# Optimization experiments

Measured on AMD Instinct MI355X. Metric: run time of the kernel, lower is better.

## Reference

```python
import jax, jax.numpy as jnp
import numpy as np

HEADS = 16
KERNEL_EPS = 1e-4  # performer_pytorch softmax_kernel eps
LN_EPS = 1e-5


def layernorm(x, g, b):
    m = jnp.mean(x, axis=-1, keepdims=True)
    v = jnp.var(x, axis=-1, keepdims=True)
    return (x - m) * jax.lax.rsqrt(v + LN_EPS) * g + b


def softmax_kernel(x, proj, is_query):
    # FAVOR+ positive random features (performer_pytorch softmax_kernel)
    d = x.shape[-1]
    m = proj.shape[0]
    xn = x * (d ** -0.25)                                   # data_normalizer * data
    dd = jnp.einsum('bhnd,md->bhnm', xn, proj)              # projected logits
    diag = 0.5 * jnp.sum(xn * xn, axis=-1, keepdims=True)   # ||x||^2/2 * normalizer^2
    if is_query:
        stab = jnp.max(dd, axis=-1, keepdims=True)
    else:
        stab = jnp.max(dd, axis=(-2, -1), keepdims=True)
    return (m ** -0.5) * (jnp.exp(dd - diag - stab) + KERNEL_EPS)


def favor_attention(x, proj, Wq, bq, Wk, bk, Wv, bv, Wo, bo):
    B, N, D = x.shape
    dh = D // HEADS

    def split(t):
        return t.reshape(B, N, HEADS, dh).transpose(0, 2, 1, 3)  # b h n d

    q = split(x @ Wq.T + bq)
    k = split(x @ Wk.T + bk)
    v = split(x @ Wv.T + bv)

    qp = softmax_kernel(q, proj, True)    # b h n m
    kp = softmax_kernel(k, proj, False)   # b h n m

    # non-causal linear attention: O(n*m*d)
    ksum = kp.sum(axis=2)                                    # b h m
    d_inv = 1.0 / jnp.einsum('bhnm,bhm->bhn', qp, ksum)      # b h n
    ctx = jnp.einsum('bhnm,bhnd->bhmd', kp, v)               # b h m d
    out = jnp.einsum('bhnm,bhmd,bhn->bhnd', qp, ctx, d_inv)  # b h n d

    out = out.transpose(0, 2, 1, 3).reshape(B, N, D)
    return out @ Wo.T + bo


def reference(x, proj, ln1_g, ln1_b, Wq, bq, Wk, bk, Wv, bv, Wo, bo,
              ln2_g, ln2_b, W1, b1, W2, b2):
    depth = proj.shape[0]
    for i in range(depth):
        h = layernorm(x, ln1_g[i], ln1_b[i])
        x = x + favor_attention(h, proj[i], Wq[i], bq[i], Wk[i], bk[i],
                                Wv[i], bv[i], Wo[i], bo[i])
        h = layernorm(x, ln2_g[i], ln2_b[i])
        x = x + (jax.nn.gelu(h @ W1[i].T + b1[i], approximate=False) @ W2[i].T + b2[i])
    return x


def _orthogonal_features(rng, m, d):
    # gaussian orthogonal random matrix, scaling=1 (rows scaled by sqrt(d))
    blocks = []
    for _ in range(m // d):
        qmat, _ = np.linalg.qr(rng.standard_normal((d, d)))
        blocks.append(qmat.T)
    return (np.sqrt(d) * np.concatenate(blocks, axis=0)).astype(np.float32)


def setup_inputs() -> dict:
    B, N, D, L, M, DH = 4, 2048, 1024, 4, 256, 64
    key = jax.random.key(0)
    ks = jax.random.split(key, 8)
    rng = np.random.default_rng(0)
    proj = jnp.asarray(np.stack([_orthogonal_features(rng, M, DH) for _ in range(L)]))
    s = 0.02
    return {
        'x': jax.random.normal(ks[0], (B, N, D), jnp.float32),
        'proj': proj,
        'ln1_g': jnp.ones((L, D), jnp.float32),
        'ln1_b': jnp.zeros((L, D), jnp.float32),
        'Wq': s * jax.random.normal(ks[1], (L, D, D), jnp.float32),
        'bq': jnp.zeros((L, D), jnp.float32),
        'Wk': s * jax.random.normal(ks[2], (L, D, D), jnp.float32),
        'bk': jnp.zeros((L, D), jnp.float32),
        'Wv': s * jax.random.normal(ks[3], (L, D, D), jnp.float32),
        'bv': jnp.zeros((L, D), jnp.float32),
        'Wo': s * jax.random.normal(ks[4], (L, D, D), jnp.float32),
        'bo': jnp.zeros((L, D), jnp.float32),
        'ln2_g': jnp.ones((L, D), jnp.float32),
        'ln2_b': jnp.zeros((L, D), jnp.float32),
        'W1': s * jax.random.normal(ks[5], (L, D, D), jnp.float32),
        'b1': jnp.zeros((L, D), jnp.float32),
        'W2': s * jax.random.normal(ks[6], (L, D, D), jnp.float32),
        'b2': jnp.zeros((L, D), jnp.float32),
    }
```

## Files before the change

kernel.cpp:

```cpp
#include <hip/hip_runtime.h>

#define B_    4
#define N_    2048
#define D_    1024
#define L_    4
#define M_    256
#define DH_   64
#define H_    16
#define BH_   64
#define ROWS_ 8192
#define WN_   1048576

typedef __bf16 bf16x8 __attribute__((ext_vector_type(8)));
typedef float  f32x4  __attribute__((ext_vector_type(4)));
typedef unsigned short u16;

__device__ __forceinline__ u16 f2b(float f){
  unsigned u = __float_as_uint(f);
  u += 0x7FFFu + ((u >> 16) & 1u);
  return (u16)(u >> 16);
}
__device__ __forceinline__ float b2f(u16 h){ return __uint_as_float(((unsigned)h) << 16); }

__device__ __forceinline__ void gload16(const u16* g, u16* l){
  __builtin_amdgcn_global_load_lds(
      (const __attribute__((address_space(1))) void*)g,
      (__attribute__((address_space(3))) void*)l, 16, 0, 0);
}

__global__ __launch_bounds__(256) void wcvt_k(const float* __restrict__ s, u16* __restrict__ d, long n){
  long i = ((long)blockIdx.x*256 + threadIdx.x)*4;
  if (i+3 < n){
    float4 v = *(const float4*)(s+i);
    d[i]=f2b(v.x); d[i+1]=f2b(v.y); d[i+2]=f2b(v.z); d[i+3]=f2b(v.w);
  } else {
    for(long j=i;j<n;j++) d[j]=f2b(s[j]);
  }
}

__global__ __launch_bounds__(256) void wcvt6_k(
    const float* __restrict__ s0, const float* __restrict__ s1,
    const float* __restrict__ s2, const float* __restrict__ s3,
    const float* __restrict__ s4, const float* __restrict__ s5,
    u16* __restrict__ dbase)
{
  int ty = blockIdx.y;
  const float* s = (ty==0)?s0:(ty==1)?s1:(ty==2)?s2:(ty==3)?s3:(ty==4)?s4:s5;
  long i = ((long)blockIdx.x*256 + threadIdx.x)*4;
  float4 v = *(const float4*)(s+i);
  long l = i >> 20, j = i & (WN_-1);
  u16* d = dbase + l*(6l*WN_) + (long)ty*WN_ + j;
  d[0]=f2b(v.x); d[1]=f2b(v.y); d[2]=f2b(v.z); d[3]=f2b(v.w);
}

__global__ void fillf_k(float* o, long n, float v){
  long i=(long)blockIdx.x*256+threadIdx.x; if(i<n) o[i]=v;
}

__global__ __launch_bounds__(256) void ln_k(const float* __restrict__ x,
    const float* __restrict__ g, const float* __restrict__ bt, u16* __restrict__ h){
  int row = blockIdx.x, t = threadIdx.x;
  const float* xr = x + (long)row*D_;
  float4 v = *(const float4*)(xr + t*4);
  float s  = v.x+v.y+v.z+v.w;
  float ss = v.x*v.x+v.y*v.y+v.z*v.z+v.w*v.w;
  #pragma unroll
  for (int m=1;m<64;m<<=1){ s += __shfl_xor(s,m); ss += __shfl_xor(ss,m); }
  __shared__ float ps[4][2];
  int w=t>>6;
  if ((t&63)==0){ ps[w][0]=s; ps[w][1]=ss; }
  __syncthreads();
  s  = ps[0][0]+ps[1][0]+ps[2][0]+ps[3][0];
  ss = ps[0][1]+ps[1][1]+ps[2][1]+ps[3][1];
  float mean = s*(1.0f/D_);
  float rs = rsqrtf(ss*(1.0f/D_) - mean*mean + 1e-5f);
  int c=t*4;
  u16* hr = h + (long)row*D_;
  hr[c+0]=f2b((v.x-mean)*rs*g[c+0]+bt[c+0]);
  hr[c+1]=f2b((v.y-mean)*rs*g[c+1]+bt[c+1]);
  hr[c+2]=f2b((v.z-mean)*rs*g[c+2]+bt[c+2]);
  hr[c+3]=f2b((v.w-mean)*rs*g[c+3]+bt[c+3]);
}

#define LOAD_PF(pF, P, w, lr, lg) \
  _Pragma("unroll") \
  for (int ni=0;ni<4;ni++) \
    _Pragma("unroll") \
    for (int ks=0;ks<2;ks++) \
      pF[ni][ks] = *(const bf16x8*)((P) + ((w)*64+ni*16+(lr))*64 + ks*32 + (lg)*8);

#define STAGE_XS_DG(Xs, X, b, hh, n0, dgL) \
  _Pragma("unroll") \
  for (int i=0;i<2;i++){ \
    int c=threadIdx.x+i*256, row=c>>3, c8=c&7; \
    uint4 dv = *(const uint4*)((X) + ((long)(b)*N_ + (n0)+row)*D_ + (hh)*DH_ + c8*8); \
    *(uint4*)((char*)(Xs) + (row<<7) + ((c8<<4)^((row&7)<<4))) = dv; \
    const u16* pe=(const u16*)&dv; \
    float sq=0.f; \
    _Pragma("unroll") \
    for (int e=0;e<8;e++){ float xv=b2f(pe[e]); sq += xv*xv; } \
    sq += __shfl_xor(sq,1); sq += __shfl_xor(sq,2); sq += __shfl_xor(sq,4); \
    if ((threadIdx.x&7)==0) (dgL)[row]=sq*0.0625f; \
  }
#define DD_MFMA_R(acc, Xs, pF, lr, lg) \
  __builtin_amdgcn_s_setprio(1); \
  _Pragma("unroll") \
  for (int ks=0;ks<2;ks++){ \
    bf16x8 aF[4]; \
    _Pragma("unroll") \
    for (int mi=0;mi<4;mi++){ \
      int row=mi*16+(lr); \
      aF[mi]=*(const bf16x8*)((const char*)(Xs) + (row<<7) + ((((ks<<2)+(lg))<<4)^((row&7)<<4))); \
    } \
    _Pragma("unroll") \
    for (int mi=0;mi<4;mi++) \
      _Pragma("unroll") \
      for (int ni=0;ni<4;ni++) \
        acc[mi][ni]=__builtin_amdgcn_mfma_f32_16x16x32_bf16(aF[mi],pF[ni][ks],acc[mi][ni],0,0,0); \
  } \
  __builtin_amdgcn_s_setprio(0);

__global__ __launch_bounds__(256) void ddctx_k(
    const u16* __restrict__ Kb, const u16* __restrict__ P,
    const u16* __restrict__ Vb,
    float* __restrict__ part, float* __restrict__ kspart,
    float* __restrict__ msl, float* __restrict__ vsl, int zoff)
{
  __shared__ __align__(16) char smem[63760];
  u16* Tr = (u16*)smem;
  u16* Xs = (u16*)(smem+36864);
  u16* Vs = (u16*)(smem+45056);
  u16* Tv = (u16*)(smem+54272);
  float* dgL = (float*)(smem+63488);
  float* rm  = (float*)(smem+63744);
  int t=threadIdx.x, w=t>>6, lane=t&63, lr=lane&15, lg=lane>>4;
  int zl=blockIdx.y, zg=zl+zoff, slot=blockIdx.x;
  int b=zg>>4, hh=zg&15;
  const float SN = 0.35355339059327373f;

  bf16x8 pF[4][2];
  LOAD_PF(pF, P, w, lr, lg);

  f32x4 cacc[4][4];
  #pragma unroll
  for (int mi=0;mi<4;mi++)
    #pragma unroll
    for (int ni=0;ni<4;ni++) cacc[mi][ni]=(f32x4){0.f,0.f,0.f,0.f};
  float ksp[4]={0.f,0.f,0.f,0.f};
  float vsacc=0.f;
  float mrun=-1e30f;

  for (int s=0;s<4;++s){
    int n0 = slot*256 + s*64;
    STAGE_XS_DG(Xs, Kb, b, hh, n0, dgL);
    {
      int row=t>>2, c16=(t&3)*16;
      const u16* src = Vb + ((long)b*N_ + n0+row)*D_ + hh*DH_ + c16;
      *(uint4*)&Tv[row*72+c16]   = *(const uint4*)src;
      *(uint4*)&Tv[row*72+c16+8] = *(const uint4*)(src+8);
    }
    __syncthreads();
    {
      int d=t>>2, nc=(t&3)*16;
      union { u16 u[16]; uint4 q[2]; } tv;
      #pragma unroll
      for (int j=0;j<16;j++) tv.u[j]=Tv[(nc+j)*72+d];
      *(uint4*)&Vs[d*72+nc]   = tv.q[0];
      *(uint4*)&Vs[d*72+nc+8] = tv.q[1];
    }
    f32x4 acc[4][4];
    #pragma unroll
    for (int mi=0;mi<4;mi++)
      #pragma unroll
      for (int ni=0;ni<4;ni++) acc[mi][ni]=(f32x4){0.f,0.f,0.f,0.f};
    DD_MFMA_R(acc, Xs, pF, lr, lg);
    {
      float mx = acc[0][0][0];
      #pragma unroll
      for (int mi=0;mi<4;mi++)
        #pragma unroll
        for (int ni=0;ni<4;ni++)
          #pragma unroll
          for (int r=0;r<4;r++) mx=fmaxf(mx,acc[mi][ni][r]);
      #pragma unroll
      for (int m=1;m<64;m<<=1) mx = fmaxf(mx, __shfl_xor(mx,m));
      if (lane==0) rm[w]=mx;
    }
    __syncthreads();
    {
      int d=t>>2, q=t&3;
      float sv=0.f;
      #pragma unroll
      for (int j=0;j<16;j++) sv += b2f(Vs[d*72+q*16+j]);
      sv += __shfl_xor(sv,1); sv += __shfl_xor(sv,2);
      if (q==0) vsacc += sv;
    }
    float dgr[16];
    #pragma unroll
    for (int mi=0;mi<4;mi++)
      #pragma unroll
      for (int r=0;r<4;r++) dgr[mi*4+r] = dgL[mi*16+lg*4+r];
    {
      float tm = SN*fmaxf(fmaxf(rm[0],rm[1]),fmaxf(rm[2],rm[3]));
      float nm = fmaxf(mrun, tm);
      float sc = __expf(mrun - nm);
      mrun = nm;
      #pragma unroll
      for (int mi=0;mi<4;mi++)
        #pragma unroll
        for (int ni=0;ni<4;ni++)
          #pragma unroll
          for (int r=0;r<4;r++) cacc[mi][ni][r] *= sc;
      #pragma unroll
      for (int ni=0;ni<4;ni++) ksp[ni] *= sc;
    }
    #pragma unroll
    for (int mi=0;mi<4;mi++)
      #pragma unroll
      for (int ni=0;ni<4;ni++){
        int col = w*64+ni*16+lr;
        u16 pk[4];
        #pragma unroll
        for (int r=0;r<4;r++){
          float kp = 0.0625f*__expf(SN*acc[mi][ni][r] - dgr[mi*4+r] - mrun);
          pk[r] = f2b(kp);
          ksp[ni] += kp;
        }
        *(uint2*)&Tr[col*72 + mi*16 + lg*4] = *(uint2*)pk;
      }
    __syncthreads();
    __builtin_amdgcn_s_setprio(1);
    #pragma unroll
    for (int ks=0;ks<2;ks++){
      bf16x8 aF[4], bF[4];
      #pragma unroll
      for (int mi=0;mi<4;mi++)
        aF[mi]=*(const bf16x8*)(Tr + (w*64+mi*16+lr)*72 + ks*32 + lg*8);
      #pragma unroll
      for (int ni=0;ni<4;ni++)
        bF[ni]=*(const bf16x8*)(Vs + (ni*16+lr)*72 + ks*32 + lg*8);
      #pragma unroll
      for (int mi=0;mi<4;mi++)
        #pragma unroll
        for (int ni=0;ni<4;ni++)
          cacc[mi][ni]=__builtin_amdgcn_mfma_f32_16x16x32_bf16(aF[mi],bF[ni],cacc[mi][ni],0,0,0);
    }
    __builtin_amdgcn_s_setprio(0);
    __syncthreads();
  }
  #pragma unroll
  for (int ni=0;ni<4;ni++){
    ksp[ni] += __shfl_xor(ksp[ni],16);
    ksp[ni] += __shfl_xor(ksp[ni],32);
  }
  long sb = (long)zl*8+slot;
  if (lane<16){
    float* kb_ = kspart + sb*256;
    #pragma unroll
    for (int ni=0;ni<4;ni++) kb_[w*64+ni*16+lane] = ksp[ni];
  }
  if (t==0) msl[sb]=mrun;
  if ((t&3)==0) vsl[sb*64 + (t>>2)] = vsacc;
  float* pb = part + sb*16384;
  #pragma unroll
  for (int mi=0;mi<4;mi++)
    #pragma unroll
    for (int ni=0;ni<4;ni++){
      int d = ni*16+lr;
      #pragma unroll
      for (int r=0;r<4;r++){
        int m = w*64+mi*16+lg*4+r;
        pb[m*64+d] = cacc[mi][ni][r];
      }
    }
}

__global__ __launch_bounds__(256) void ctxred2_k(
    const float* __restrict__ part, const float* __restrict__ kspart,
    const float* __restrict__ msl, const float* __restrict__ vsl,
    u16* __restrict__ ctxT, float* __restrict__ ksm)
{
  int q = blockIdx.x, z = blockIdx.y, t = threadIdx.x;
  const float* pz = part + (long)z*8*16384;
  const float* kz = kspart + (long)z*8*256;
  const float* mz = msl + (long)z*8;
  const float* vz = vsl + (long)z*8*64;
  float mg = mz[0];
  #pragma unroll
  for (int s8=1;s8<8;s8++) mg = fmaxf(mg, mz[s8]);
  float scl[8];
  #pragma unroll
  for (int s8=0;s8<8;s8++) scl[s8] = __expf(mz[s8]-mg);
  __shared__ float vsT[64];
  if (t<64){
    float vv=0.f;
    #pragma unroll
    for (int s8=0;s8<8;s8++) vv += vz[s8*64+t];
    vsT[t]=vv;
  }
  __syncthreads();
  int ml = t&63, dg = t>>6;
  int m  = q*64 + ml;
  f32x4 r4[4];
  #pragma unroll
  for (int j=0;j<4;j++) r4[j]=(f32x4){0.f,0.f,0.f,0.f};
  #pragma unroll
  for (int s8=0;s8<8;s8++){
    const float* ps = pz + (long)s8*16384 + (long)m*64 + dg*16;
    float sc = scl[s8];
    #pragma unroll
    for (int j=0;j<4;j++){
      f32x4 v = *(const f32x4*)(ps + j*4);
      r4[j] += (f32x4){sc*v[0],sc*v[1],sc*v[2],sc*v[3]};
    }
  }
  if (dg==0){
    float s=0.f;
    #pragma unroll
    for (int s8=0;s8<8;s8++) s += kz[s8*256+m]*scl[s8];
    ksm[(long)z*256+m] = s + 0.0128f;
  }
  __shared__ __align__(16) u16 TT[64][72];
  #pragma unroll
  for (int j=0;j<4;j++)
    #pragma unroll
    for (int e=0;e<4;e++){
      int d = dg*16 + j*4 + e;
      TT[d][ml] = f2b(r4[j][e] + 6.25e-6f*vsT[d]);
    }
  __syncthreads();
  int d = t>>2, ms=(t&3)*16;
  union { u16 u[16]; uint4 qq[2]; } tmp;
  #pragma unroll
  for (int j=0;j<16;j++) tmp.u[j]=TT[d][ms+j];
  u16* co = ctxT + (long)z*16384 + d*256 + q*64 + ms;
  *(uint4*)co     = tmp.qq[0];
  *(uint4*)(co+8) = tmp.qq[1];
}

__global__ __launch_bounds__(256) void ddq_attn_k(
    const u16* __restrict__ Qb, const u16* __restrict__ P,
    const float* __restrict__ ksm, const u16* __restrict__ ctxT,
    u16* __restrict__ at, int zoff)
{
  __shared__ __align__(16) char smem[46336];
  u16*   qpL = (u16*)smem;
  float* rdot= (float*)(smem+33792);
  float* dnvs= (float*)(smem+34816);
  u16*   Xs  = (u16*)(smem+36864);
  float* rm  = (float*)(smem+45056);
  float* dgL = (float*)(smem+46080);
  int t=threadIdx.x, w=t>>6, lane=t&63, lr=lane&15, lg=lane>>4;
  int zl=blockIdx.y, zg=zl+zoff, n0=blockIdx.x*64;
  int b=zg>>4, hh=zg&15;
  const float SN = 0.35355339059327373f;

  bf16x8 pF[4][2];
  LOAD_PF(pF, P, w, lr, lg);
  STAGE_XS_DG(Xs, Qb, b, hh, n0, dgL);
  __syncthreads();
  f32x4 acc[4][4];
  #pragma unroll
  for (int mi=0;mi<4;mi++)
    #pragma unroll
    for (int ni=0;ni<4;ni++) acc[mi][ni]=(f32x4){0.f,0.f,0.f,0.f};
  DD_MFMA_R(acc, Xs, pF, lr, lg);
  float rmx[4][4];
  #pragma unroll
  for (int mi=0;mi<4;mi++)
    #pragma unroll
    for (int r=0;r<4;r++){
      float v = acc[mi][0][r];
      #pragma unroll
      for (int ni=1;ni<4;ni++) v=fmaxf(v, acc[mi][ni][r]);
      #pragma unroll
      for (int m=1;m<16;m<<=1) v = fmaxf(v, __shfl_xor(v,m));
      rmx[mi][r]=v;
    }
  if (lr==0){
    #pragma unroll
    for (int mi=0;mi<4;mi++)
      #pragma unroll
      for (int r=0;r<4;r++) rm[w*64 + mi*16 + lg*4 + r] = rmx[mi][r];
  }
  __syncthreads();
  float dgr[16];
  #pragma unroll
  for (int mi=0;mi<4;mi++)
    #pragma unroll
    for (int r=0;r<4;r++) dgr[mi*4+r] = dgL[mi*16+lg*4+r];
  const float* ksz = ksm + (long)zl*256;
  float kcol[4];
  #pragma unroll
  for (int ni=0;ni<4;ni++) kcol[ni] = ksz[w*64+ni*16+lr];
  float rd[4][4];
  #pragma unroll
  for (int mi=0;mi<4;mi++)
    #pragma unroll
    for (int r=0;r<4;r++){
      int rw = mi*16+lg*4+r;
      float st = fmaxf(fmaxf(rm[rw],rm[64+rw]),fmaxf(rm[128+rw],rm[192+rw]));
      float dgv = dgr[mi*4+r];
      float rsum = 0.f;
      #pragma unroll
      for (int ni=0;ni<4;ni++){
        int col = w*64+ni*16+lr;
        float qpv = 0.0625f*(__expf(SN*acc[mi][ni][r] - dgv - SN*st) + 1e-4f);
        qpL[rw*264+col] = f2b(qpv);
        rsum += qpv*kcol[ni];
      }
      rd[mi][r]=rsum;
    }
  #pragma unroll
  for (int mi=0;mi<4;mi++)
    #pragma unroll
    for (int r=0;r<4;r++){
      #pragma unroll
      for (int m=1;m<16;m<<=1) rd[mi][r] += __shfl_xor(rd[mi][r],m);
    }
  if (lr==0){
    #pragma unroll
    for (int mi=0;mi<4;mi++)
      #pragma unroll
      for (int r=0;r<4;r++) rdot[w*64 + mi*16+lg*4+r] = rd[mi][r];
  }
  __syncthreads();
  if (t<64) dnvs[t] = 1.0f/(rdot[t]+rdot[64+t]+rdot[128+t]+rdot[192+t]);
  __syncthreads();
  const u16* cz = ctxT + (long)zl*16384;
  f32x4 aacc[4];
  #pragma unroll
  for (int ni=0;ni<4;ni++) aacc[ni]=(f32x4){0.f,0.f,0.f,0.f};
  __builtin_amdgcn_s_setprio(1);
  #pragma unroll
  for (int ks=0;ks<8;ks++){
    bf16x8 aF = *(const bf16x8*)(qpL + (w*16+lr)*264 + ks*32 + lg*8);
    #pragma unroll
    for (int ni=0;ni<4;ni++){
      bf16x8 bF = *(const bf16x8*)(cz + (ni*16+lr)*256 + ks*32 + lg*8);
      aacc[ni]=__builtin_amdgcn_mfma_f32_16x16x32_bf16(aF,bF,aacc[ni],0,0,0);
    }
  }
  __builtin_amdgcn_s_setprio(0);
  #pragma unroll
  for (int ni=0;ni<4;ni++){
    #pragma unroll
    for (int r=0;r<4;r++){
      int n = n0 + w*16 + lg*4 + r;
      at[((long)b*N_ + n)*D_ + hh*64 + ni*16 + lr] = f2b(aacc[ni][r]*dnvs[w*16+lg*4+r]);
    }
  }
}

template<int EPI,bool XS>
__global__ __launch_bounds__(512,2) void gemm3_k(
    const u16* __restrict__ A, int lda,
    const u16* __restrict__ W, int ldw,
    const float* __restrict__ bias, const float* __restrict__ biasK, const float* __restrict__ biasV,
    void* __restrict__ Cv, int ldc, int K)
{
  constexpr int BM=256, BN=128;
  extern __shared__ __align__(16) u16 lds3[];
  u16* AsB = lds3;
  u16* BsB = lds3 + 3*BM*64;
  int t=threadIdx.x;
  int bx, by;
  if (XS){
    unsigned gx=gridDim.x, flat=blockIdx.y*gx+blockIdx.x;
    unsigned cpx=(gx*gridDim.y)>>3;
    unsigned s=(flat&7)*cpx + (flat>>3);
    bx = s % gx; by = s / gx;
  } else { bx = blockIdx.x; by = blockIdx.y; }
  const u16* Ab = A + (long)by*BM*lda;
  const u16* Wb = W + (long)bx*BN*ldw;
  int w=t>>6, lane=t&63, lr=lane&15, lg=lane>>4;
  int wr=w>>1, wc=w&1;
  int srow=lane>>3, swcol=((lane&7)^srow)*8;
  f32x4 acc[4][4];
  #pragma unroll
  for (int mi=0;mi<4;mi++)
    #pragma unroll
    for (int ni=0;ni<4;ni++) acc[mi][ni]=(f32x4){0.f,0.f,0.f,0.f};

  auto stage=[&](int kt, int sbuf){
    const u16* Ak = Ab + kt*64;
    u16* Ad = AsB + sbuf*(BM*64);
    #pragma unroll
    for (int i=0;i<4;i++){
      int rb=w*32+i*8;
      gload16(Ak + (long)(rb+srow)*lda + swcol, Ad + rb*64);
    }
    const u16* Bk = Wb + kt*64;
    u16* Bd = BsB + sbuf*(BN*64);
    #pragma unroll
    for (int i=0;i<2;i++){
      int rb=w*16+i*8;
      gload16(Bk + (long)(rb+srow)*ldw + swcol, Bd + rb*64);
    }
  };

  const int nK = K/64;
  stage(0,0); if (nK>1) stage(1,1);
  int rbuf=0, sbuf=2;
  for (int kt=0; kt<nK; ++kt){
    if (kt+1<nK) asm volatile("s_waitcnt vmcnt(6)" ::: "memory");
    else         asm volatile("s_waitcnt vmcnt(0)" ::: "memory");
    __builtin_amdgcn_s_barrier();
    if (kt+2<nK) stage(kt+2, sbuf);
    const u16* Al = AsB + rbuf*(BM*64);
    const u16* Bl = BsB + rbuf*(BN*64);
    bf16x8 aF[4][2], bF[4][2];
    #pragma unroll
    for (int ni=0;ni<4;ni++){
      int row=wc*64+ni*16+lr;
      #pragma unroll
      for (int ks=0;ks<2;ks++)
        bF[ni][ks]=*(const bf16x8*)((const char*)Bl + (row<<7) + ((((ks<<2)+lg)<<4)^((row&7)<<4)));
    }
    #pragma unroll
    for (int mi=0;mi<4;mi++){
      int row=wr*64+mi*16+lr;
      #pragma unroll
      for (int ks=0;ks<2;ks++)
        aF[mi][ks]=*(const bf16x8*)((const char*)Al + (row<<7) + ((((ks<<2)+lg)<<4)^((row&7)<<4)));
    }
    #pragma unroll
    for (int ks=0;ks<2;ks++)
      #pragma unroll
      for (int mi=0;mi<4;mi++)
        #pragma unroll
        for (int ni=0;ni<4;ni++)
          acc[mi][ni]=__builtin_amdgcn_mfma_f32_16x16x32_bf16(aF[mi][ks],bF[ni][ks],acc[mi][ni],0,0,0);
    rbuf = (rbuf==2)?0:rbuf+1;
    sbuf = (sbuf==2)?0:sbuf+1;
  }

  #pragma unroll
  for (int mi=0;mi<4;mi++){
    #pragma unroll
    for (int ni=0;ni<4;ni++){
      int col = bx*BN + wc*64 + ni*16 + lr;
      float bv = 0.0f;
      if (EPI==6){
        int seg = col>>10;
        const float* bp = (seg==0)?bias:((seg==1)?biasK:biasV);
        bv = bp[col&1023];
      } else {
        bv = bias[col];
      }
      #pragma unroll
      for (int r=0;r<4;r++){
        int row = by*BM + wr*64 + mi*16 + lg*4 + r;
        float v = acc[mi][ni][r];
        if (EPI==1){
          ((float*)Cv)[(long)row*ldc + col] += v+bv;
        } else if (EPI==2){
          float u=v+bv;
          ((u16*)Cv)[(long)row*ldc + col] = f2b(0.5f*u*(1.0f+erff(u*0.70710678118654752f)));
        } else {
          int seg = col>>10, c = col&1023;
          ((u16*)Cv)[(long)seg*((long)ROWS_*D_) + (long)row*D_ + c] = f2b(v+bv);
        }
      }
    }
  }
}

struct WS {
  u16 *wbuf, *pjb, *hb, *qb, *kb, *pbuf, *sh16, *ctxT;
  float *part, *kspart, *msl, *vsl, *ksm;
  size_t total;
};
static WS plan_ws(char* base, int allW, int CH){
  WS w; size_t off=0;
  auto al=[&](size_t b)->char*{ char* p=base+off; off=(off+b+255)&~(size_t)255; return p; };
  const size_t TB=(size_t)ROWS_*D_*2;
  w.wbuf=(u16*)al((allW?6ull*L_:6ull)*WN_*2);
  w.pjb =(u16*)al((size_t)L_*M_*DH_*2);
  w.hb  =(u16*)al(TB);
  w.qb  =(u16*)al(TB);
  w.kb  =(u16*)al(TB);
  w.pbuf=(u16*)al(TB);
  w.sh16=(u16*)al(TB);
  w.part=(float*)al((size_t)CH*8*M_*DH_*4);
  w.kspart=(float*)al((size_t)CH*8*M_*4);
  w.msl =(float*)al((size_t)CH*8*4);
  w.vsl =(float*)al((size_t)CH*8*DH_*4);
  w.ctxT=(u16*)al((size_t)BH_*DH_*M_*2);
  w.ksm =(float*)al((size_t)BH_*M_*4);
  w.total=off;
  return w;
}

extern "C" void kernel_launch(void* const* d_in, const int* in_sizes, int n_in,
                              void* d_out, int out_size, void* d_ws, size_t ws_size,
                              hipStream_t stream)
{
  const float* x    = (const float*)d_in[0];
  const float* proj = (const float*)d_in[1];
  const float* ln1g = (const float*)d_in[2];
  const float* ln1b = (const float*)d_in[3];
  const float* Wq   = (const float*)d_in[4];
  const float* bq   = (const float*)d_in[5];
  const float* Wk   = (const float*)d_in[6];
  const float* bk   = (const float*)d_in[7];
  const float* Wv   = (const float*)d_in[8];
  const float* bv   = (const float*)d_in[9];
  const float* Wo   = (const float*)d_in[10];
  const float* bo   = (const float*)d_in[11];
  const float* ln2g = (const float*)d_in[12];
  const float* ln2b = (const float*)d_in[13];
  const float* W1   = (const float*)d_in[14];
  const float* b1   = (const float*)d_in[15];
  const float* W2   = (const float*)d_in[16];
  const float* b2   = (const float*)d_in[17];

  char* base=(char*)d_ws;
  int allW=1, CH=64;
  WS w = plan_ws(base, 1, 64);
  if (w.total > ws_size){ CH=16; w = plan_ws(base, 1, 16); }
  if (w.total > ws_size){ allW=0; w = plan_ws(base, 0, 16); }
  if (w.total > ws_size){
    fillf_k<<<(out_size+255)/256,256,0,stream>>>((float*)d_out,(long)out_size,(float)(ws_size>>20));
    return;
  }
  const int NCH = BH_/CH;

  u16* vb = w.pbuf;
  u16* at = w.hb;
  u16* tm = w.sh16;

  wcvt_k<<<(L_*M_*DH_/4+255)/256,256,0,stream>>>(proj,w.pjb,(long)L_*M_*DH_);
  if (allW){
    const long na = (long)L_*WN_;
    const int g2 = (int)(na/4/256);
    wcvt6_k<<<dim3(g2,6),256,0,stream>>>(Wq,Wk,Wv,Wo,W1,W2, w.wbuf);
  }
  hipMemcpyAsync(d_out, x, (size_t)ROWS_*D_*4, hipMemcpyDeviceToDevice, stream);
  float* Xc = (float*)d_out;

  const long wn = (long)WN_;
  const int wg = (int)(wn/4/256);
  const size_t G3LDS = 3ull*(256+128)*64*2;
  dim3 gBig(D_/128, ROWS_/256, 1);
  dim3 gQKV(3*D_/128, ROWS_/256, 1);

  for (int l=0;l<L_;l++){
    u16* lw = w.wbuf + (allW ? (size_t)l*6*wn : 0);
    u16* wqkv=lw;  u16* wo=lw+3*wn;  u16* w1=lw+4*wn;  u16* w2=lw+5*wn;
    if (!allW){
      wcvt_k<<<wg,256,0,stream>>>(Wq+(size_t)l*wn,lw,wn);
      wcvt_k<<<wg,256,0,stream>>>(Wk+(size_t)l*wn,lw+wn,wn);
      wcvt_k<<<wg,256,0,stream>>>(Wv+(size_t)l*wn,lw+2*wn,wn);
      wcvt_k<<<wg,256,0,stream>>>(Wo+(size_t)l*wn,wo,wn);
      wcvt_k<<<wg,256,0,stream>>>(W1+(size_t)l*wn,w1,wn);
      wcvt_k<<<wg,256,0,stream>>>(W2+(size_t)l*wn,w2,wn);
    }
    const u16* pj = w.pjb + (size_t)l*M_*DH_;

    ln_k<<<ROWS_,256,0,stream>>>(Xc, ln1g+(size_t)l*D_, ln1b+(size_t)l*D_, w.hb);
    gemm3_k<6,true><<<gQKV,512,G3LDS,stream>>>(w.hb,D_, wqkv,D_,
        bq+(size_t)l*D_, bk+(size_t)l*D_, bv+(size_t)l*D_, w.qb,D_,D_);

    for (int ch=0; ch<NCH; ch++){
      int zoff = ch*CH;
      ddctx_k<<<dim3(8,CH),256,0,stream>>>(w.kb, pj, vb, w.part, w.kspart,
                                           w.msl, w.vsl, zoff);
      ctxred2_k<<<dim3(4,CH),256,0,stream>>>(w.part, w.kspart, w.msl, w.vsl,
                                     w.ctxT+(long)zoff*DH_*M_, w.ksm+(long)zoff*M_);
      ddq_attn_k<<<dim3(N_/64,CH),256,0,stream>>>(w.qb, pj,
                                                  w.ksm+(long)zoff*M_,
                                                  w.ctxT+(long)zoff*DH_*M_, at, zoff);
    }

    gemm3_k<1,true><<<gBig,512,G3LDS,stream>>>(at,D_, wo,D_,
        bo+(size_t)l*D_, nullptr, nullptr, Xc,D_,D_);
    ln_k<<<ROWS_,256,0,stream>>>(Xc, ln2g+(size_t)l*D_, ln2b+(size_t)l*D_, w.hb);
    gemm3_k<2,true><<<gBig,512,G3LDS,stream>>>(w.hb,D_, w1,D_,
        b1+(size_t)l*D_, nullptr, nullptr, tm,D_,D_);
    gemm3_k<1,true><<<gBig,512,G3LDS,stream>>>(tm,D_, w2,D_,
        b2+(size_t)l*D_, nullptr, nullptr, Xc,D_,D_);
  }
}
```

Baseline: 1.149 ms.

## Remap GEMM warp tiling to 2x4 and interleave prefetch with MFMA phases

```diff
diff --git a/kernel.cpp b/kernel.cpp
--- a/kernel.cpp
+++ b/kernel.cpp
@@ -474,72 +474,85 @@
   const u16* Ab = A + (long)by*BM*lda;
   const u16* Wb = W + (long)bx*BN*ldw;
   int w=t>>6, lane=t&63, lr=lane&15, lg=lane>>4;
-  int wr=w>>1, wc=w&1;
+  int wr=w>>2, wc=w&3;
   int srow=lane>>3, swcol=((lane&7)^srow)*8;
-  f32x4 acc[4][4];
-  #pragma unroll
-  for (int mi=0;mi<4;mi++)
-    #pragma unroll
-    for (int ni=0;ni<4;ni++) acc[mi][ni]=(f32x4){0.f,0.f,0.f,0.f};
-
-  auto stage=[&](int kt, int sbuf){
-    const u16* Ak = Ab + kt*64;
-    u16* Ad = AsB + sbuf*(BM*64);
-    #pragma unroll
-    for (int i=0;i<4;i++){
-      int rb=w*32+i*8;
-      gload16(Ak + (long)(rb+srow)*lda + swcol, Ad + rb*64);
-    }
-    const u16* Bk = Wb + kt*64;
-    u16* Bd = BsB + sbuf*(BN*64);
-    #pragma unroll
-    for (int i=0;i<2;i++){
-      int rb=w*16+i*8;
-      gload16(Bk + (long)(rb+srow)*ldw + swcol, Bd + rb*64);
+  f32x4 acc[8][2];
+  #pragma unroll
+  for (int mi=0;mi<8;mi++)
+    #pragma unroll
+    for (int ni=0;ni<2;ni++) acc[mi][ni]=(f32x4){0.f,0.f,0.f,0.f};
+
+  auto stagePc=[&](int kt, int sbuf, int pc){
+    if (pc<2){
+      const u16* Ak = Ab + kt*64;
+      u16* Ad = AsB + sbuf*(BM*64);
+      #pragma unroll
+      for (int i=0;i<2;i++){
+        int rb=w*32+(pc*2+i)*8;
+        gload16(Ak + (long)(rb+srow)*lda + swcol, Ad + rb*64);
+      }
+    } else {
+      const u16* Bk = Wb + kt*64;
+      u16* Bd = BsB + sbuf*(BN*64);
+      #pragma unroll
+      for (int i=0;i<2;i++){
+        int rb=w*16+i*8;
+        gload16(Bk + (long)(rb+srow)*ldw + swcol, Bd + rb*64);
+      }
     }
   };
 
   const int nK = K/64;
-  stage(0,0); if (nK>1) stage(1,1);
+  { stagePc(0,0,0); stagePc(0,0,1); stagePc(0,0,2); }
+  if (nK>1){ stagePc(1,1,0); stagePc(1,1,1); stagePc(1,1,2); }
   int rbuf=0, sbuf=2;
   for (int kt=0; kt<nK; ++kt){
     if (kt+1<nK) asm volatile("s_waitcnt vmcnt(6)" ::: "memory");
     else         asm volatile("s_waitcnt vmcnt(0)" ::: "memory");
     __builtin_amdgcn_s_barrier();
-    if (kt+2<nK) stage(kt+2, sbuf);
     const u16* Al = AsB + rbuf*(BM*64);
     const u16* Bl = BsB + rbuf*(BN*64);
-    bf16x8 aF[4][2], bF[4][2];
-    #pragma unroll
-    for (int ni=0;ni<4;ni++){
-      int row=wc*64+ni*16+lr;
+    bf16x8 bF[2][2];
+    #pragma unroll
+    for (int ni=0;ni<2;ni++){
+      int row=wc*32+ni*16+lr;
       #pragma unroll
       for (int ks=0;ks<2;ks++)
         bF[ni][ks]=*(const bf16x8*)((const char*)Bl + (row<<7) + ((((ks<<2)+lg)<<4)^((row&7)<<4)));
     }
-    #pragma unroll
-    for (int mi=0;mi<4;mi++){
-      int row=wr*64+mi*16+lr;
+    bool pf = (kt+2<nK);
+    #pragma unroll
+    for (int q=0;q<4;q++){
+      bf16x8 aF[2][2];
+      #pragma unroll
+      for (int dm=0;dm<2;dm++){
+        int row=wr*128+(q*2+dm)*16+lr;
+        #pragma unroll
+        for (int ks=0;ks<2;ks++)
+          aF[dm][ks]=*(const bf16x8*)((const char*)Al + (row<<7) + ((((ks<<2)+lg)<<4)^((row&7)<<4)));
+      }
+      if (q<3 && pf) stagePc(kt+2, sbuf, q);
+      __builtin_amdgcn_s_barrier();
+      __builtin_amdgcn_s_setprio(1);
       #pragma unroll
       for (int ks=0;ks<2;ks++)
-        aF[mi][ks]=*(const bf16x8*)((const char*)Al + (row<<7) + ((((ks<<2)+lg)<<4)^((row&7)<<4)));
-    }
-    #pragma unroll
-    for (int ks=0;ks<2;ks++)
-      #pragma unroll
-      for (int mi=0;mi<4;mi++)
         #pragma unroll
-        for (int ni=0;ni<4;ni++)
-          acc[mi][ni]=__builtin_amdgcn_mfma_f32_16x16x32_bf16(aF[mi][ks],bF[ni][ks],acc[mi][ni],0,0,0);
+        for (int dm=0;dm<2;dm++)
+          #pragma unroll
+          for (int ni=0;ni<2;ni++)
+            acc[q*2+dm][ni]=__builtin_amdgcn_mfma_f32_16x16x32_bf16(aF[dm][ks],bF[ni][ks],acc[q*2+dm][ni],0,0,0);
+      __builtin_amdgcn_s_setprio(0);
+      __builtin_amdgcn_s_barrier();
+    }
     rbuf = (rbuf==2)?0:rbuf+1;
     sbuf = (sbuf==2)?0:sbuf+1;
   }
 
   #pragma unroll
-  for (int mi=0;mi<4;mi++){
-    #pragma unroll
-    for (int ni=0;ni<4;ni++){
-      int col = bx*BN + wc*64 + ni*16 + lr;
+  for (int mi=0;mi<8;mi++){
+    #pragma unroll
+    for (int ni=0;ni<2;ni++){
+      int col = bx*BN + wc*32 + ni*16 + lr;
       float bv = 0.0f;
       if (EPI==6){
         int seg = col>>10;
@@ -550,7 +563,7 @@
       }
       #pragma unroll
       for (int r=0;r<4;r++){
-        int row = by*BM + wr*64 + mi*16 + lg*4 + r;
+        int row = by*BM + wr*128 + mi*16 + lg*4 + r;
         float v = acc[mi][ni][r];
         if (EPI==1){
           ((float*)Cv)[(long)row*ldc + col] += v+bv;
```

Result: slower. 1.211 ms (+5.4%).
